# Performance work log

Measured on AMD Instinct MI355X. Metric: run time of the kernel, lower is better.

## Reference

```python
import jax, jax.numpy as jnp
import numpy as np

EPS = 1e-5  # BatchNorm eps (inference-mode BN with running stats)


def bn(x, g, b, m, v):
    # x: [B,C,H,W]; per-channel affine BN (inference)
    inv = jax.lax.rsqrt(v + EPS)
    return (x - m[None, :, None, None]) * (g * inv)[None, :, None, None] + b[None, :, None, None]


def conv1x1(x, w):
    # x: [B,Ci,H,W], w: [Co,Ci,1,1]
    return jnp.einsum('bchw,oc->bohw', x, w[:, :, 0, 0])


def conv3x3(x, w, b):
    out = jax.lax.conv_general_dilated(
        x, w, window_strides=(1, 1), padding=((1, 1), (1, 1)),
        dimension_numbers=('NCHW', 'OIHW', 'NCHW'))
    return out + b[None, :, None, None]


def deform_conv3x3(x, offset, w):
    # x: [B,C,H,W]; offset: [B,18,H,W] with channel 2k = dy_k, 2k+1 = dx_k
    # w: [Co,C,3,3]; stride=1, pad=1, dilation=1, deformable_groups=1
    B, C, H, W = x.shape
    K = 9
    kidx = jnp.arange(K)
    kdy = (kidx // 3 - 1).astype(x.dtype)  # base kernel y offsets in {-1,0,1}
    kdx = (kidx % 3 - 1).astype(x.dtype)
    off = offset.reshape(B, K, 2, H, W)
    gh = jnp.arange(H, dtype=x.dtype)
    gw = jnp.arange(W, dtype=x.dtype)
    # sampling locations [B,K,H,W]
    py = gh[None, None, :, None] + kdy[None, :, None, None] + off[:, :, 0]
    px = gw[None, None, None, :] + kdx[None, :, None, None] + off[:, :, 1]

    y0 = jnp.floor(py)
    x0 = jnp.floor(px)
    wy1 = py - y0
    wx1 = px - x0
    y0i = y0.astype(jnp.int32)
    x0i = x0.astype(jnp.int32)

    xflat = x.reshape(B, C, H * W)

    def gather(yi, xi):
        valid = ((yi >= 0) & (yi < H) & (xi >= 0) & (xi < W))
        idx = (jnp.clip(yi, 0, H - 1) * W + jnp.clip(xi, 0, W - 1)).reshape(B, 1, -1)
        g = jnp.take_along_axis(xflat, idx, axis=2).reshape(B, C, K, H, W)
        return g * valid[:, None].astype(x.dtype)

    sampled = (
        gather(y0i, x0i) * ((1 - wy1) * (1 - wx1))[:, None]
        + gather(y0i, x0i + 1) * ((1 - wy1) * wx1)[:, None]
        + gather(y0i + 1, x0i) * (wy1 * (1 - wx1))[:, None]
        + gather(y0i + 1, x0i + 1) * (wy1 * wx1)[:, None]
    )  # [B,C,K,H,W]
    return jnp.einsum('bckhw,ock->bohw', sampled, w.reshape(w.shape[0], C, K))


def setup_inputs() -> dict:
    key = jax.random.key(0)
    ks = jax.random.split(key, 20)
    B, Cin, H, W = 2, 1024, 64, 64
    Cb, Cout = 256, 1024

    def msra(k, shape):
        fan_out = shape[0] * int(np.prod(shape[2:]))
        return jax.random.normal(k, shape, jnp.float32) * np.sqrt(2.0 / fan_out)

    inp = {
        'x': jax.random.normal(ks[0], (B, Cin, H, W), jnp.float32),
        'w1': msra(ks[1], (Cb, Cin, 1, 1)),
        'g1': jnp.ones((Cb,)), 'b1': jnp.zeros((Cb,)),
        'm1': jax.random.normal(ks[2], (Cb,)) * 0.1,
        'v1': jax.random.uniform(ks[3], (Cb,)) + 0.5,
        # offset conv (small weights so offsets stay in a realistic range)
        'w_off': msra(ks[4], (18, Cb, 3, 3)) * 0.05,
        'b_off': jnp.zeros((18,)),
        'w2': msra(ks[5], (Cb, Cb, 3, 3)),
        'g2': jnp.ones((Cb,)), 'b2': jnp.zeros((Cb,)),
        'm2': jax.random.normal(ks[6], (Cb,)) * 0.1,
        'v2': jax.random.uniform(ks[7], (Cb,)) + 0.5,
        'w3': msra(ks[8], (Cout, Cb, 1, 1)),
        'g3': jnp.ones((Cout,)), 'b3': jnp.zeros((Cout,)),
        'm3': jax.random.normal(ks[9], (Cout,)) * 0.1,
        'v3': jax.random.uniform(ks[10], (Cout,)) + 0.5,
    }
    return inp


def reference(x, w1, g1, b1, m1, v1, w_off, b_off, w2, g2, b2, m2, v2,
              w3, g3, b3, m3, v3):
    out = jax.nn.relu(bn(conv1x1(x, w1), g1, b1, m1, v1))
    offset = conv3x3(out, w_off, b_off)          # [B,18,H,W]
    out = bn(deform_conv3x3(out, offset, w2), g2, b2, m2, v2)
    out = jax.nn.relu(out)
    out = bn(conv1x1(out, w3), g3, b3, m3, v3)
    out = out + x                                 # identity shortcut (Cin==Cout, stride=1)
    return jax.nn.relu(out)
```

## Files before the change

kernel.cpp:

```cpp
#include <hip/hip_runtime.h>
#include <hip/hip_bf16.h>

#define EPSV 1e-5f

typedef __attribute__((ext_vector_type(4))) float f32x4;
typedef __attribute__((ext_vector_type(8))) short bf16x8;
typedef unsigned short u16;
typedef unsigned int u32;

#define AS1(p) ((const __attribute__((address_space(1))) void*)(p))
#define AS3(p) ((__attribute__((address_space(3))) void*)(p))

__device__ __forceinline__ float bf2f(u16 u) {
    union { u32 i; float f; } x; x.i = ((u32)u) << 16; return x.f;
}
__device__ __forceinline__ u16 f2bf(float f) {
    __hip_bfloat16 h = __float2bfloat16(f);
    return *reinterpret_cast<u16*>(&h);
}

__global__ __launch_bounds__(256) void prep_all(
    const float* __restrict__ w1, const float* __restrict__ w3,
    const float* __restrict__ w_off, const float* __restrict__ w2,
    u16* __restrict__ wb1, u16* __restrict__ wb3,
    u16* __restrict__ wOffP, u16* __restrict__ wb2d,
    u16* __restrict__ zbuf)
{
    const int bz  = blockIdx.x;
    const int tid = threadIdx.x;
    if (bz < 512) {
        int i = bz * 256 + tid;
        const float* src; u16* dst; int j;
        if (i < 65536) { src = w1; dst = wb1; j = i; }
        else           { src = w3; dst = wb3; j = i - 65536; }
        float4 v = ((const float4*)src)[j];
        ushort4 o;
        o.x = f2bf(v.x); o.y = f2bf(v.y); o.z = f2bf(v.z); o.w = f2bf(v.w);
        ((ushort4*)dst)[j] = o;
        return;
    }
    const int bz1 = bz - 512;
    if (bz1 == 136) { ((u32*)zbuf)[tid] = 0; return; }
    if (bz1 < 64) {
#pragma unroll
        for (int k = 0; k < 9; k++) {
            float v = (bz1 < 18) ? w_off[((size_t)(bz1 * 256 + tid)) * 9 + k] : 0.f;
            wOffP[(size_t)bz1 * 2304 + k * 256 + tid] = f2bf(v);
        }
        return;
    }
    const int bz2 = bz1 - 64;
    const int set = bz2 % 18;
    const int kz  = bz2 / 18;
    const int tap = set >> 1, hk = set & 1;
#pragma unroll
    for (int j = 0; j < 4; j++) {
        bf16x8 ov;
#pragma unroll
        for (int kk = 0; kk < 8; kk++) {
            const int ch = kz * 64 + hk * 32 + j * 8 + kk;
            ov[kk] = (short)f2bf(w2[((size_t)(tid * 256 + ch)) * 9 + tap]);
        }
        *(bf16x8*)(wb2d + ((size_t)(bz2 * 4 + j)) * 2048 + tid * 8) = ov;
    }
}

__global__ __launch_bounds__(256) void cvt_x_T(const float* __restrict__ x,
                                               u16* __restrict__ xbT) {
    __shared__ u16 tile[64][72];
    const int tid = threadIdx.x;
    const int hw0 = blockIdx.x << 6;
    const int c0  = blockIdx.y << 6;
    const int b   = blockIdx.z;
    const int cl  = tid >> 4;
    const int hwl = (tid & 15) << 2;
#pragma unroll
    for (int i = 0; i < 4; i++) {
        const int c = cl + i * 16;
        float4 v = *(const float4*)(x + (((size_t)(b * 1024 + c0 + c)) << 12) + hw0 + hwl);
        tile[hwl + 0][c] = f2bf(v.x);
        tile[hwl + 1][c] = f2bf(v.y);
        tile[hwl + 2][c] = f2bf(v.z);
        tile[hwl + 3][c] = f2bf(v.w);
    }
    __syncthreads();
    const int hw  = tid >> 2;
    const int seg = tid & 3;
    u16* dst = xbT + ((size_t)(b * 4096 + hw0 + hw)) * 1024 + c0 + seg * 16;
    const u16* src = &tile[hw][seg * 16];
#pragma unroll
    for (int q = 0; q < 2; q++)
        *(uint4*)(dst + q * 8) = *(const uint4*)(src + q * 8);
}

#define MFMA8(ASP, BSP)                                                          \
    do {                                                                         \
        bf16x8 a0 = *(const bf16x8*)(ASP);                                       \
        bf16x8 a1 = *(const bf16x8*)((ASP) + 512);                               \
        bf16x8 b0 = *(const bf16x8*)(BSP);                                       \
        bf16x8 b1 = *(const bf16x8*)((BSP) + 512);                               \
        bf16x8 b2 = *(const bf16x8*)((BSP) + 1024);                              \
        bf16x8 b3 = *(const bf16x8*)((BSP) + 1536);                              \
        acc[0][0] = __builtin_amdgcn_mfma_f32_16x16x32_bf16(a0, b0, acc[0][0], 0, 0, 0); \
        acc[0][1] = __builtin_amdgcn_mfma_f32_16x16x32_bf16(a0, b1, acc[0][1], 0, 0, 0); \
        acc[0][2] = __builtin_amdgcn_mfma_f32_16x16x32_bf16(a0, b2, acc[0][2], 0, 0, 0); \
        acc[0][3] = __builtin_amdgcn_mfma_f32_16x16x32_bf16(a0, b3, acc[0][3], 0, 0, 0); \
        acc[1][0] = __builtin_amdgcn_mfma_f32_16x16x32_bf16(a1, b0, acc[1][0], 0, 0, 0); \
        acc[1][1] = __builtin_amdgcn_mfma_f32_16x16x32_bf16(a1, b1, acc[1][1], 0, 0, 0); \
        acc[1][2] = __builtin_amdgcn_mfma_f32_16x16x32_bf16(a1, b2, acc[1][2], 0, 0, 0); \
        acc[1][3] = __builtin_amdgcn_mfma_f32_16x16x32_bf16(a1, b3, acc[1][3], 0, 0, 0); \
    } while (0)

#define WAIT_BAR()                                  \
    do {                                            \
        asm volatile("s_waitcnt vmcnt(3)" ::: "memory"); \
        __builtin_amdgcn_s_barrier();               \
        __builtin_amdgcn_sched_barrier(0);          \
    } while (0)

#define POST_BAR()                                  \
    do {                                            \
        __builtin_amdgcn_s_barrier();               \
        __builtin_amdgcn_sched_barrier(0);          \
    } while (0)

template<int MODE>
__global__ __launch_bounds__(256) void gemm_bn(
    const u16* __restrict__ A, const u16* __restrict__ BT,
    const float* __restrict__ g, const float* __restrict__ bb,
    const float* __restrict__ m, const float* __restrict__ v,
    const float* __restrict__ resid, void* __restrict__ out, int K, int Ksub)
{
    extern __shared__ char sm[];

    const int tid  = threadIdx.x;
    const int lane = tid & 63;
    const int wid  = tid >> 6;
    const int n0 = blockIdx.x << 7;
    const int m0 = blockIdx.y << 6;
    const int kBase = blockIdx.z * Ksub;
    const int wr = wid >> 1, wc = wid & 1;
    const int lr = lane & 15, kg = lane >> 4;

    f32x4 acc[2][4] = {};

    const int arow = tid >> 2, aseg = (tid & 3) << 3;
    const u16* aG  = A  + (size_t)(m0 + arow) * K + kBase + aseg;
    const u16* bG0 = BT + (size_t)(n0 + arow) * K + kBase + aseg;
    const u16* bG1 = BT + (size_t)(n0 + 64 + arow) * K + kBase + aseg;

    char* ldsA0  = sm + wid * 1024;
    char* ldsA1  = sm + 4096  + wid * 1024;
    char* ldsB00 = sm + 8192  + wid * 1024;
    char* ldsB01 = sm + 12288 + wid * 1024;
    char* ldsB10 = sm + 16384 + wid * 1024;
    char* ldsB11 = sm + 20480 + wid * 1024;

    const u16* Asp0 = (const u16*)(sm)         + (wr * 32 + lr) * 32 + kg * 8;
    const u16* Asp1 = (const u16*)(sm + 4096)  + (wr * 32 + lr) * 32 + kg * 8;
    const u16* Bsp0 = (const u16*)(sm + 8192)  + (wc * 64 + lr) * 32 + kg * 8;
    const u16* Bsp1 = (const u16*)(sm + 16384) + (wc * 64 + lr) * 32 + kg * 8;

    float sc[2][4], tc[2][4];
#pragma unroll
    for (int mm = 0; mm < 2; mm++)
#pragma unroll
        for (int r = 0; r < 4; r++) {
            const int o = m0 + wr * 32 + mm * 16 + kg * 4 + r;
            const float s = g[o] * rsqrtf(v[o] + EPSV);
            sc[mm][r] = s;
            tc[mm][r] = bb[o] - m[o] * s;
        }
    asm volatile("s_waitcnt vmcnt(0) lgkmcnt(0)" ::: "memory");
    __builtin_amdgcn_sched_barrier(0);

#define ISSUE_G(LA, LB0, LB1, kt)                                                  \
    do {                                                                           \
        __builtin_amdgcn_global_load_lds(AS1(aG + (kt)),  AS3(LA),  16, 0, 0);     \
        __builtin_amdgcn_global_load_lds(AS1(bG0 + (kt)), AS3(LB0), 16, 0, 0);     \
        __builtin_amdgcn_global_load_lds(AS1(bG1 + (kt)), AS3(LB1), 16, 0, 0);     \
    } while (0)

    const int nT = Ksub >> 5;
    ISSUE_G(ldsA0, ldsB00, ldsB01, 0);
    ISSUE_G(ldsA1, ldsB10, ldsB11, 32);

    for (int t = 0; t < nT; t += 2) {
        WAIT_BAR();
        MFMA8(Asp0, Bsp0);
        POST_BAR();
        { const int kn = (t + 2 < nT ? t + 2 : t) << 5;
          ISSUE_G(ldsA0, ldsB00, ldsB01, kn); }
        WAIT_BAR();
        MFMA8(Asp1, Bsp1);
        POST_BAR();
        { const int kn = (t + 3 < nT ? t + 3 : t + 1) << 5;
          ISSUE_G(ldsA1, ldsB10, ldsB11, kn); }
    }
#undef ISSUE_G

    if (MODE == 1) {
        u32* T32 = (u32*)(sm + 24576);
#pragma unroll
        for (int mm = 0; mm < 2; mm++) {
            const int ol = wr * 32 + mm * 16 + kg * 4;
            const int cw0 = ol >> 1;
#pragma unroll
            for (int j = 0; j < 4; j++) {
                const int nl = wc * 64 + j * 16 + lr;
                const int sw = (nl >> 3) & 3;
                float v0 = acc[mm][j][0] * sc[mm][0] + tc[mm][0];
                float v1 = acc[mm][j][1] * sc[mm][1] + tc[mm][1];
                float v2 = acc[mm][j][2] * sc[mm][2] + tc[mm][2];
                float v3 = acc[mm][j][3] * sc[mm][3] + tc[mm][3];
                v0 = v0 > 0.f ? v0 : 0.f; v1 = v1 > 0.f ? v1 : 0.f;
                v2 = v2 > 0.f ? v2 : 0.f; v3 = v3 > 0.f ? v3 : 0.f;
                uint2 pw;
                pw.x = (u32)f2bf(v0) | ((u32)f2bf(v1) << 16);
                pw.y = (u32)f2bf(v2) | ((u32)f2bf(v3) << 16);
                *(uint2*)&T32[nl * 36 + (cw0 ^ (sw << 2))] = pw;
            }
        }
        __syncthreads();
        const int nl = tid >> 1, half = tid & 1;
        const int sw = (nl >> 3) & 3;
        u16* dst = (u16*)out + (size_t)(n0 + nl) * 256 + m0 + half * 32;
#pragma unroll
        for (int q = 0; q < 4; q++) {
            uint4 val = *(const uint4*)&T32[nl * 36 + ((half * 16 + q * 4) ^ (sw << 2))];
            *(uint4*)(dst + q * 8) = val;
        }
    } else {
        float* T = (float*)(sm + 24576);
#pragma unroll
        for (int mm = 0; mm < 2; mm++) {
            const int ol = wr * 32 + mm * 16 + kg * 4;
#pragma unroll
            for (int j = 0; j < 4; j++) {
                const int nl = wc * 64 + j * 16 + lr;
#pragma unroll
                for (int r = 0; r < 4; r++)
                    T[(ol + r) * 132 + nl] = acc[mm][j][r] * sc[mm][r] + tc[mm][r];
            }
        }
        __syncthreads();
        float* O = (float*)out;
        for (int idx = tid; idx < 2048; idx += 256) {
            const int ol  = idx >> 5;
            const int nl4 = (idx & 31) << 2;
            const int n = n0 + nl4;
            const size_t gidx = ((size_t)(n >> 12) << 22) + ((size_t)(m0 + ol) << 12) + (n & 4095);
            float4 rv = *(const float4*)(resid + gidx);
            float4 ov;
            ov.x = T[ol * 132 + nl4 + 0] + rv.x;
            ov.y = T[ol * 132 + nl4 + 1] + rv.y;
            ov.z = T[ol * 132 + nl4 + 2] + rv.z;
            ov.w = T[ol * 132 + nl4 + 3] + rv.w;
            ov.x = ov.x > 0.f ? ov.x : 0.f;
            ov.y = ov.y > 0.f ? ov.y : 0.f;
            ov.z = ov.z > 0.f ? ov.z : 0.f;
            ov.w = ov.w > 0.f ? ov.w : 0.f;
            *(float4*)(O + gidx) = ov;
        }
    }
}

__global__ __launch_bounds__(256) void gemm_off(
    const u16* __restrict__ A,
    const u16* __restrict__ out1T,
    const u16* __restrict__ zbuf,
    float* __restrict__ offsP)
{
    __shared__ char sm[24576];

    const int tid  = threadIdx.x;
    const int lane = tid & 63;
    const int wid  = tid >> 6;
    const int n0 = blockIdx.x << 7;
    const int kz = blockIdx.y;
    const int wr = wid >> 1, wc = wid & 1;
    const int lr = lane & 15, kg = lane >> 4;

    f32x4 acc[2][4] = {};

    const int arow = tid >> 2, aseg = (tid & 3) << 3;
    const u16* aG = A + (size_t)arow * 2304 + aseg;
    const int nB0 = n0 + arow, nB1 = n0 + 64 + arow;
    const int y0r = (nB0 & 4095) >> 6, x0r = nB0 & 63;
    const int y1r = (nB1 & 4095) >> 6, x1r = nB1 & 63;

    char* ldsA0  = sm + wid * 1024;
    char* ldsA1  = sm + 4096  + wid * 1024;
    char* ldsB00 = sm + 8192  + wid * 1024;
    char* ldsB01 = sm + 12288 + wid * 1024;
    char* ldsB10 = sm + 16384 + wid * 1024;
    char* ldsB11 = sm + 20480 + wid * 1024;

    const u16* Asp0 = (const u16*)(sm)         + (wr * 32 + lr) * 32 + kg * 8;
    const u16* Asp1 = (const u16*)(sm + 4096)  + (wr * 32 + lr) * 32 + kg * 8;
    const u16* Bsp0 = (const u16*)(sm + 8192)  + (wc * 64 + lr) * 32 + kg * 8;
    const u16* Bsp1 = (const u16*)(sm + 16384) + (wc * 64 + lr) * 32 + kg * 8;

#define ISSUE_O(LA, LB0, LB1, kt)                                                  \
    do {                                                                           \
        const int tap = (kt) >> 8, c0 = (kt) & 255;                                \
        const int dy = tap / 3 - 1, dx = tap % 3 - 1;                              \
        const int sh = dy * 64 + dx;                                               \
        const bool vv0 = ((unsigned)(y0r + dy) < 64u) && ((unsigned)(x0r + dx) < 64u); \
        const bool vv1 = ((unsigned)(y1r + dy) < 64u) && ((unsigned)(x1r + dx) < 64u); \
        const u16* s0 = vv0 ? out1T + (size_t)(nB0 + sh) * 256 + c0 + aseg : zbuf + aseg; \
        const u16* s1 = vv1 ? out1T + (size_t)(nB1 + sh) * 256 + c0 + aseg : zbuf + aseg; \
        __builtin_amdgcn_global_load_lds(AS1(aG + (kt)), AS3(LA),  16, 0, 0);      \
        __builtin_amdgcn_global_load_lds(AS1(s0),        AS3(LB0), 16, 0, 0);      \
        __builtin_amdgcn_global_load_lds(AS1(s1),        AS3(LB1), 16, 0, 0);      \
    } while (0)

    const int kBase = kz * 384;
    ISSUE_O(ldsA0, ldsB00, ldsB01, kBase);
    ISSUE_O(ldsA1, ldsB10, ldsB11, kBase + 32);

    for (int t = 0; t < 12; t += 2) {
        WAIT_BAR();
        MFMA8(Asp0, Bsp0);
        POST_BAR();
        { const int kn = kBase + ((t + 2 < 12 ? t + 2 : t) << 5);
          ISSUE_O(ldsA0, ldsB00, ldsB01, kn); }
        WAIT_BAR();
        MFMA8(Asp1, Bsp1);
        POST_BAR();
        { const int kn = kBase + ((t + 3 < 12 ? t + 3 : t + 1) << 5);
          ISSUE_O(ldsA1, ldsB10, ldsB11, kn); }
    }
#undef ISSUE_O

    asm volatile("s_waitcnt vmcnt(0)" ::: "memory");

#pragma unroll
    for (int mm = 0; mm < 2; mm++)
#pragma unroll
        for (int r = 0; r < 4; r++) {
            const int o = wr * 32 + mm * 16 + kg * 4 + r;
            if (o < 18) {
#pragma unroll
                for (int j = 0; j < 4; j++) {
                    const int n = n0 + wc * 64 + j * 16 + lr;
                    offsP[(size_t)kz * 147456 +
                          (((size_t)((n >> 12) * 18 + o)) << 12) + (n & 4095)] =
                        acc[mm][j][r];
                }
            }
        }
}

__global__ __launch_bounds__(256) void gemm_def(
    const u16* __restrict__ wb2d,
    const u16* __restrict__ out1T,
    const float* __restrict__ offsP,
    const float* __restrict__ b_off,
    u16* __restrict__ P)
{
    extern __shared__ char sm[];
    char*   ldsB0 = sm;
    char*   ldsB1 = sm + 4160;
    int4*   s_ofs = (int4*)(sm + 8320);
    float4* s_w   = (float4*)(sm + 17536);

    const int tid  = threadIdx.x;
    const int lane = tid & 63;
    const int wid  = tid >> 6;
    const int n0 = blockIdx.x << 6;
    const int kz = blockIdx.y;
    const int b  = n0 >> 12;
    const int h  = (n0 >> 6) & 63;
    const int lr = lane & 15, kg = lane >> 4;

    for (int p = tid; p < 576; p += 256) {
        const int t   = p >> 6;
        const int nl_ = p & 63;
        const size_t iy = (((size_t)(b * 18 + 2 * t)) << 12) + (h << 6) + nl_;
        float dy = b_off[2 * t], dx = b_off[2 * t + 1];
#pragma unroll
        for (int kzz = 0; kzz < 6; kzz++) {
            dy += offsP[(size_t)kzz * 147456 + iy];
            dx += offsP[(size_t)kzz * 147456 + iy + 4096];
        }
        const float py = (float)h + (float)(t / 3 - 1) + dy;
        const float px = (float)nl_ + (float)(t % 3 - 1) + dx;
        const float y0f = floorf(py), x0f = floorf(px);
        const int y0 = (int)y0f, x0 = (int)x0f;
        const float wy1 = py - y0f, wx1 = px - x0f;
        const float wy0 = 1.f - wy1, wx0 = 1.f - wx1;
        const int y1 = y0 + 1, x1 = x0 + 1;
        const bool vy0 = (y0 >= 0) && (y0 < 64);
        const bool vy1 = (y1 >= 0) && (y1 < 64);
        const bool vx0 = (x0 >= 0) && (x0 < 64);
        const bool vx1 = (x1 >= 0) && (x1 < 64);
        const int cy0 = min(max(y0, 0), 63), cy1 = min(max(y1, 0), 63);
        const int cx0 = min(max(x0, 0), 63), cx1 = min(max(x1, 0), 63);
        const int rb = b << 12;
        int4 o4; float4 w4;
        o4.x = (rb + (cy0 << 6) + cx0) << 9;  w4.x = wy0 * wx0 * ((vy0 && vx0) ? 1.f : 0.f);
        o4.y = (rb + (cy0 << 6) + cx1) << 9;  w4.y = wy0 * wx1 * ((vy0 && vx1) ? 1.f : 0.f);
        o4.z = (rb + (cy1 << 6) + cx0) << 9;  w4.z = wy1 * wx0 * ((vy1 && vx0) ? 1.f : 0.f);
        o4.w = (rb + (cy1 << 6) + cx1) << 9;  w4.w = wy1 * wx1 * ((vy1 && vx1) ? 1.f : 0.f);
        s_ofs[nl_ * 9 + t] = o4; s_w[nl_ * 9 + t] = w4;
    }
    __syncthreads();

    const int nl = tid >> 2;
    const int q  = tid & 3;
    const u16* aSet  = wb2d + (size_t)(kz * 18) * 8192 + kg * 2048
                            + (wid * 64 + lr) * 8;
    const char* o1B = (const char*)out1T;
    const int cbQ = kz * 128 + q * 16;

    f32x4 acc[4][4] = {};
    bf16x8 av0[4], av1[4], cr0[4], cr1[4];

#define PWC(p_) ((p_) < 18 ? (p_) : 17)

#define LOADA(RI, pt_)                                                             \
    do {                                                                           \
        const u16* ag_ = aSet + (size_t)(pt_) * 8192;                              \
        av##RI[0] = *(const bf16x8*)(ag_);                                         \
        av##RI[1] = *(const bf16x8*)(ag_ + 128);                                   \
        av##RI[2] = *(const bf16x8*)(ag_ + 256);                                   \
        av##RI[3] = *(const bf16x8*)(ag_ + 384);                                   \
    } while (0)

#define LOADC(RI, pt_)                                                             \
    do {                                                                           \
        const int tap_ = (pt_) >> 1, hk_ = (pt_) & 1;                              \
        const int4 o4_ = s_ofs[nl * 9 + tap_];                                     \
        const int cb_ = cbQ + hk_ * 64;                                            \
        cr##RI[0] = *(const bf16x8*)(o1B + o4_.x + cb_);                           \
        cr##RI[1] = *(const bf16x8*)(o1B + o4_.y + cb_);                           \
        cr##RI[2] = *(const bf16x8*)(o1B + o4_.z + cb_);                           \
        cr##RI[3] = *(const bf16x8*)(o1B + o4_.w + cb_);                           \
    } while (0)

#define PACKB(RI, LB, pw_)                                                         \
    do {                                                                           \
        const float4 w4_ = s_w[nl * 9 + ((pw_) >> 1)];                             \
        bf16x8 pk_;                                                                \
        _Pragma("unroll")                                                          \
        for (int i_ = 0; i_ < 8; i_++) {                                           \
            const float f_ = w4_.x * bf2f((u16)cr##RI[0][i_])                      \
                           + w4_.y * bf2f((u16)cr##RI[1][i_])                      \
                           + w4_.z * bf2f((u16)cr##RI[2][i_])                      \
                           + w4_.w * bf2f((u16)cr##RI[3][i_]);                     \
            pk_[i_] = (short)f2bf(f_);                                             \
        }                                                                          \
        *(bf16x8*)((LB) + q * 1040 + nl * 16) = pk_;                               \
    } while (0)

#define MFMA16(AV, LB)                                                             \
    do {                                                                           \
        bf16x8 bv0 = *(const bf16x8*)((LB) + kg * 1040 + ( 0 + lr) * 16);          \
        bf16x8 bv1 = *(const bf16x8*)((LB) + kg * 1040 + (16 + lr) * 16);          \
        bf16x8 bv2 = *(const bf16x8*)((LB) + kg * 1040 + (32 + lr) * 16);          \
        bf16x8 bv3 = *(const bf16x8*)((LB) + kg * 1040 + (48 + lr) * 16);          \
        acc[0][0] = __builtin_amdgcn_mfma_f32_16x16x32_bf16(AV[0], bv0, acc[0][0], 0, 0, 0); \
        acc[0][1] = __builtin_amdgcn_mfma_f32_16x16x32_bf16(AV[0], bv1, acc[0][1], 0, 0, 0); \
        acc[0][2] = __builtin_amdgcn_mfma_f32_16x16x32_bf16(AV[0], bv2, acc[0][2], 0, 0, 0); \
        acc[0][3] = __builtin_amdgcn_mfma_f32_16x16x32_bf16(AV[0], bv3, acc[0][3], 0, 0, 0); \
        acc[1][0] = __builtin_amdgcn_mfma_f32_16x16x32_bf16(AV[1], bv0, acc[1][0], 0, 0, 0); \
        acc[1][1] = __builtin_amdgcn_mfma_f32_16x16x32_bf16(AV[1], bv1, acc[1][1], 0, 0, 0); \
        acc[1][2] = __builtin_amdgcn_mfma_f32_16x16x32_bf16(AV[1], bv2, acc[1][2], 0, 0, 0); \
        acc[1][3] = __builtin_amdgcn_mfma_f32_16x16x32_bf16(AV[1], bv3, acc[1][3], 0, 0, 0); \
        acc[2][0] = __builtin_amdgcn_mfma_f32_16x16x32_bf16(AV[2], bv0, acc[2][0], 0, 0, 0); \
        acc[2][1] = __builtin_amdgcn_mfma_f32_16x16x32_bf16(AV[2], bv1, acc[2][1], 0, 0, 0); \
        acc[2][2] = __builtin_amdgcn_mfma_f32_16x16x32_bf16(AV[2], bv2, acc[2][2], 0, 0, 0); \
        acc[2][3] = __builtin_amdgcn_mfma_f32_16x16x32_bf16(AV[2], bv3, acc[2][3], 0, 0, 0); \
        acc[3][0] = __builtin_amdgcn_mfma_f32_16x16x32_bf16(AV[3], bv0, acc[3][0], 0, 0, 0); \
        acc[3][1] = __builtin_amdgcn_mfma_f32_16x16x32_bf16(AV[3], bv1, acc[3][1], 0, 0, 0); \
        acc[3][2] = __builtin_amdgcn_mfma_f32_16x16x32_bf16(AV[3], bv2, acc[3][2], 0, 0, 0); \
        acc[3][3] = __builtin_amdgcn_mfma_f32_16x16x32_bf16(AV[3], bv3, acc[3][3], 0, 0, 0); \
    } while (0)

#define END_BAR()                                   \
    do {                                            \
        asm volatile("s_waitcnt lgkmcnt(0)" ::: "memory"); \
        __builtin_amdgcn_s_barrier();               \
        __builtin_amdgcn_sched_barrier(0);          \
    } while (0)

    LOADC(0, 0); LOADA(0, 0);
    LOADC(1, 1); LOADA(1, 1);
    PACKB(0, ldsB0, 0);
    LOADC(0, 2);
    END_BAR();

    for (int t = 0; t < 18; t += 2) {
        PACKB(1, ldsB1, PWC(t + 1));
        LOADC(1, PWC(t + 3));
        MFMA16(av0, ldsB0);
        LOADA(0, PWC(t + 2));
        END_BAR();
        PACKB(0, ldsB0, PWC(t + 2));
        LOADC(0, PWC(t + 4));
        MFMA16(av1, ldsB1);
        LOADA(1, PWC(t + 3));
        END_BAR();
    }
#undef END_BAR
#undef MFMA16
#undef PACKB
#undef LOADC
#undef LOADA
#undef PWC

    u16* Pk = P + (size_t)kz * 2097152;
#pragma unroll
    for (int mf = 0; mf < 4; mf++)
#pragma unroll
        for (int r = 0; r < 4; r++) {
            const int o = wid * 64 + mf * 16 + kg * 4 + r;
#pragma unroll
            for (int nf = 0; nf < 4; nf++) {
                const int n = n0 + nf * 16 + lr;
                Pk[((size_t)o << 13) + n] = f2bf(acc[mf][nf][r]);
            }
        }
}

__global__ __launch_bounds__(256) void reduce_bn(
    const u16* __restrict__ P,
    const float* __restrict__ g, const float* __restrict__ bb,
    const float* __restrict__ m, const float* __restrict__ v,
    u16* __restrict__ o2T)
{
    __shared__ u16 tile[64][72];
    const int tid = threadIdx.x;
    const int n0 = blockIdx.x << 6;
    const int m0 = blockIdx.y << 6;

    const int ml = tid >> 2;
    const int ns = (tid & 3) << 4;
    const int o = m0 + ml;
    const float s = g[o] * rsqrtf(v[o] + EPSV);
    const float tcv = bb[o] - m[o] * s;
    const size_t base = ((size_t)o << 13) + n0 + ns;
#pragma unroll
    for (int qq = 0; qq < 2; qq++) {
        bf16x8 a = *(const bf16x8*)(P + base + qq * 8);
        bf16x8 b = *(const bf16x8*)(P + 2097152 + base + qq * 8);
        bf16x8 c = *(const bf16x8*)(P + 2 * 2097152 + base + qq * 8);
        bf16x8 d = *(const bf16x8*)(P + 3 * 2097152 + base + qq * 8);
#pragma unroll
        for (int i = 0; i < 8; i++) {
            float f = (bf2f((u16)a[i]) + bf2f((u16)b[i])
                     + bf2f((u16)c[i]) + bf2f((u16)d[i])) * s + tcv;
            f = f > 0.f ? f : 0.f;
            tile[ns + qq * 8 + i][ml] = f2bf(f);
        }
    }
    __syncthreads();
    const int nl = tid >> 2, seg = tid & 3;
    u16* dst = o2T + (size_t)(n0 + nl) * 256 + m0 + seg * 16;
    const u16* src = &tile[nl][seg * 16];
#pragma unroll
    for (int qq = 0; qq < 2; qq++)
        *(uint4*)(dst + qq * 8) = *(const uint4*)(src + qq * 8);
}

extern "C" void kernel_launch(void* const* d_in, const int* in_sizes, int n_in,
                              void* d_out, int out_size, void* d_ws, size_t ws_size,
                              hipStream_t stream) {
    const float* x     = (const float*)d_in[0];
    const float* w1    = (const float*)d_in[1];
    const float* g1    = (const float*)d_in[2];
    const float* b1    = (const float*)d_in[3];
    const float* m1    = (const float*)d_in[4];
    const float* v1    = (const float*)d_in[5];
    const float* w_off = (const float*)d_in[6];
    const float* b_off = (const float*)d_in[7];
    const float* w2    = (const float*)d_in[8];
    const float* g2    = (const float*)d_in[9];
    const float* b2    = (const float*)d_in[10];
    const float* m2    = (const float*)d_in[11];
    const float* v2    = (const float*)d_in[12];
    const float* w3    = (const float*)d_in[13];
    const float* g3    = (const float*)d_in[14];
    const float* b3    = (const float*)d_in[15];
    const float* m3    = (const float*)d_in[16];
    const float* v3    = (const float*)d_in[17];
    float* out = (float*)d_out;

    char* ws = (char*)d_ws;
    u16*  xbT   = (u16*)ws;   ws += (size_t)8192 * 1024 * 2;
    u16*  wb1   = (u16*)ws;   ws += (size_t)256 * 1024 * 2;
    u16*  wb3   = (u16*)ws;   ws += (size_t)1024 * 256 * 2;
    u16*  wOffP = (u16*)ws;   ws += (size_t)64 * 2304 * 2;
    u16*  wb2d  = (u16*)ws;   ws += (size_t)72 * 8192 * 2;
    u16*  zbuf  = (u16*)ws;   ws += (size_t)512 * 2;
    u16*  out1T = (u16*)ws;   ws += (size_t)8192 * 256 * 2;
    float* offsP = (float*)ws; ws += (size_t)6 * 147456 * 4;
    u16*  o2T   = (u16*)ws;   ws += (size_t)8192 * 256 * 2;
    u16*  P     = (u16*)ws;   ws += (size_t)4 * 2097152 * 2;

    prep_all<<<dim3(649), 256, 0, stream>>>(w1, w3, w_off, w2,
                                            wb1, wb3, wOffP, wb2d, zbuf);
    cvt_x_T<<<dim3(64, 16, 2), 256, 0, stream>>>(x, xbT);

    gemm_bn<1><<<dim3(64, 4), 256, 24576 + 18432, stream>>>(
        wb1, xbT, g1, b1, m1, v1, nullptr, out1T, 1024, 1024);

    gemm_off<<<dim3(64, 6), 256, 0, stream>>>(wOffP, out1T, zbuf, offsP);

    gemm_def<<<dim3(128, 4), 256, 26752, stream>>>(wb2d, out1T, offsP, b_off, P);

    reduce_bn<<<dim3(128, 4), 256, 0, stream>>>(P, g2, b2, m2, v2, o2T);

    gemm_bn<2><<<dim3(64, 16), 256, 24576 + 64 * 132 * 4, stream>>>(
        wb3, o2T, g3, b3, m3, v3, x, out, 256, 256);
}
```

Measured before the change: 92.93 us.

## Process full tap per pipeline stage in deformable GEMM, halving barriers

The deformable-conv GEMM pipeline now handles a whole kernel tap (both 64-channel halves) per stage instead of half a tap. This halves the number of LDS double-buffer stages and barriers (9 instead of 18) and issues twice as many gathers per stage for more memory-level parallelism. In exchange it doubles the register footprint for the A and gathered values and grows LDS from about 26 KB to 35 KB, which may lower occupancy.

Result: slower. 95.54 us (+2.8%).

```diff
diff --git a/kernel.cpp b/kernel.cpp
--- a/kernel.cpp
+++ b/kernel.cpp
@@ -361,9 +361,9 @@
 {
     extern __shared__ char sm[];
     char*   ldsB0 = sm;
-    char*   ldsB1 = sm + 4160;
-    int4*   s_ofs = (int4*)(sm + 8320);
-    float4* s_w   = (float4*)(sm + 17536);
+    char*   ldsB1 = sm + 8320;
+    int4*   s_ofs = (int4*)(sm + 16640);
+    float4* s_w   = (float4*)(sm + 25856);
 
     const int tid  = threadIdx.x;
     const int lane = tid & 63;
@@ -415,51 +415,64 @@
     const int cbQ = kz * 128 + q * 16;
 
     f32x4 acc[4][4] = {};
-    bf16x8 av0[4], av1[4], cr0[4], cr1[4];
-
-#define PWC(p_) ((p_) < 18 ? (p_) : 17)
-
-#define LOADA(RI, pt_)                                                             \
-    do {                                                                           \
-        const u16* ag_ = aSet + (size_t)(pt_) * 8192;                              \
-        av##RI[0] = *(const bf16x8*)(ag_);                                         \
-        av##RI[1] = *(const bf16x8*)(ag_ + 128);                                   \
-        av##RI[2] = *(const bf16x8*)(ag_ + 256);                                   \
-        av##RI[3] = *(const bf16x8*)(ag_ + 384);                                   \
-    } while (0)
-
-#define LOADC(RI, pt_)                                                             \
-    do {                                                                           \
-        const int tap_ = (pt_) >> 1, hk_ = (pt_) & 1;                              \
-        const int4 o4_ = s_ofs[nl * 9 + tap_];                                     \
-        const int cb_ = cbQ + hk_ * 64;                                            \
-        cr##RI[0] = *(const bf16x8*)(o1B + o4_.x + cb_);                           \
-        cr##RI[1] = *(const bf16x8*)(o1B + o4_.y + cb_);                           \
-        cr##RI[2] = *(const bf16x8*)(o1B + o4_.z + cb_);                           \
-        cr##RI[3] = *(const bf16x8*)(o1B + o4_.w + cb_);                           \
-    } while (0)
-
-#define PACKB(RI, LB, pw_)                                                         \
-    do {                                                                           \
-        const float4 w4_ = s_w[nl * 9 + ((pw_) >> 1)];                             \
+    bf16x8 av0a[4], av0b[4], av1a[4], av1b[4];
+    bf16x8 cr0a[4], cr0b[4], cr1a[4], cr1b[4];
+
+#define PWC(p_) ((p_) < 9 ? (p_) : 8)
+
+#define LOADA(RI, P_)                                                              \
+    do {                                                                           \
+        const u16* ag_ = aSet + (size_t)(2 * (P_)) * 8192;                         \
+        av##RI##a[0] = *(const bf16x8*)(ag_);                                      \
+        av##RI##a[1] = *(const bf16x8*)(ag_ + 128);                                \
+        av##RI##a[2] = *(const bf16x8*)(ag_ + 256);                                \
+        av##RI##a[3] = *(const bf16x8*)(ag_ + 384);                                \
+        av##RI##b[0] = *(const bf16x8*)(ag_ + 8192);                               \
+        av##RI##b[1] = *(const bf16x8*)(ag_ + 8320);                               \
+        av##RI##b[2] = *(const bf16x8*)(ag_ + 8448);                               \
+        av##RI##b[3] = *(const bf16x8*)(ag_ + 8576);                               \
+    } while (0)
+
+#define LOADC(RI, P_)                                                              \
+    do {                                                                           \
+        const int4 o4_ = s_ofs[nl * 9 + (P_)];                                     \
+        cr##RI##a[0] = *(const bf16x8*)(o1B + o4_.x + cbQ);                        \
+        cr##RI##a[1] = *(const bf16x8*)(o1B + o4_.y + cbQ);                        \
+        cr##RI##a[2] = *(const bf16x8*)(o1B + o4_.z + cbQ);                        \
+        cr##RI##a[3] = *(const bf16x8*)(o1B + o4_.w + cbQ);                        \
+        cr##RI##b[0] = *(const bf16x8*)(o1B + o4_.x + cbQ + 64);                   \
+        cr##RI##b[1] = *(const bf16x8*)(o1B + o4_.y + cbQ + 64);                   \
+        cr##RI##b[2] = *(const bf16x8*)(o1B + o4_.z + cbQ + 64);                   \
+        cr##RI##b[3] = *(const bf16x8*)(o1B + o4_.w + cbQ + 64);                   \
+    } while (0)
+
+#define PACK1(CR, LBP)                                                             \
+    do {                                                                           \
         bf16x8 pk_;                                                                \
         _Pragma("unroll")                                                          \
         for (int i_ = 0; i_ < 8; i_++) {                                           \
-            const float f_ = w4_.x * bf2f((u16)cr##RI[0][i_])                      \
-                           + w4_.y * bf2f((u16)cr##RI[1][i_])                      \
-                           + w4_.z * bf2f((u16)cr##RI[2][i_])                      \
-                           + w4_.w * bf2f((u16)cr##RI[3][i_]);                     \
+            const float f_ = w4_.x * bf2f((u16)CR[0][i_])                          \
+                           + w4_.y * bf2f((u16)CR[1][i_])                          \
+                           + w4_.z * bf2f((u16)CR[2][i_])                          \
+                           + w4_.w * bf2f((u16)CR[3][i_]);                         \
             pk_[i_] = (short)f2bf(f_);                                             \
         }                                                                          \
-        *(bf16x8*)((LB) + q * 1040 + nl * 16) = pk_;                               \
-    } while (0)
-
-#define MFMA16(AV, LB)                                                             \
-    do {                                                                           \
-        bf16x8 bv0 = *(const bf16x8*)((LB) + kg * 1040 + ( 0 + lr) * 16);          \
-        bf16x8 bv1 = *(const bf16x8*)((LB) + kg * 1040 + (16 + lr) * 16);          \
-        bf16x8 bv2 = *(const bf16x8*)((LB) + kg * 1040 + (32 + lr) * 16);          \
-        bf16x8 bv3 = *(const bf16x8*)((LB) + kg * 1040 + (48 + lr) * 16);          \
+        *(bf16x8*)(LBP) = pk_;                                                     \
+    } while (0)
+
+#define PACKB(RI, LB, P_)                                                          \
+    do {                                                                           \
+        const float4 w4_ = s_w[nl * 9 + (P_)];                                     \
+        PACK1(cr##RI##a, (LB) + q * 1040 + nl * 16);                               \
+        PACK1(cr##RI##b, (LB) + 4160 + q * 1040 + nl * 16);                        \
+    } while (0)
+
+#define MFMA16S(AV, LBS)                                                           \
+    do {                                                                           \
+        bf16x8 bv0 = *(const bf16x8*)((LBS) + kg * 1040 + ( 0 + lr) * 16);         \
+        bf16x8 bv1 = *(const bf16x8*)((LBS) + kg * 1040 + (16 + lr) * 16);         \
+        bf16x8 bv2 = *(const bf16x8*)((LBS) + kg * 1040 + (32 + lr) * 16);         \
+        bf16x8 bv3 = *(const bf16x8*)((LBS) + kg * 1040 + (48 + lr) * 16);         \
         acc[0][0] = __builtin_amdgcn_mfma_f32_16x16x32_bf16(AV[0], bv0, acc[0][0], 0, 0, 0); \
         acc[0][1] = __builtin_amdgcn_mfma_f32_16x16x32_bf16(AV[0], bv1, acc[0][1], 0, 0, 0); \
         acc[0][2] = __builtin_amdgcn_mfma_f32_16x16x32_bf16(AV[0], bv2, acc[0][2], 0, 0, 0); \
@@ -478,6 +491,12 @@
         acc[3][3] = __builtin_amdgcn_mfma_f32_16x16x32_bf16(AV[3], bv3, acc[3][3], 0, 0, 0); \
     } while (0)
 
+#define MFMA32(RI, LB)                                                             \
+    do {                                                                           \
+        MFMA16S(av##RI##a, (LB));                                                  \
+        MFMA16S(av##RI##b, (LB) + 4160);                                           \
+    } while (0)
+
 #define END_BAR()                                   \
     do {                                            \
         asm volatile("s_waitcnt lgkmcnt(0)" ::: "memory"); \
@@ -491,21 +510,24 @@
     LOADC(0, 2);
     END_BAR();
 
-    for (int t = 0; t < 18; t += 2) {
+    for (int t = 0; t < 8; t += 2) {
         PACKB(1, ldsB1, PWC(t + 1));
         LOADC(1, PWC(t + 3));
-        MFMA16(av0, ldsB0);
+        MFMA32(0, ldsB0);
         LOADA(0, PWC(t + 2));
         END_BAR();
         PACKB(0, ldsB0, PWC(t + 2));
         LOADC(0, PWC(t + 4));
-        MFMA16(av1, ldsB1);
+        MFMA32(1, ldsB1);
         LOADA(1, PWC(t + 3));
         END_BAR();
     }
+    MFMA32(0, ldsB0);
 #undef END_BAR
-#undef MFMA16
+#undef MFMA32
+#undef MFMA16S
 #undef PACKB
+#undef PACK1
 #undef LOADC
 #undef LOADA
 #undef PWC
@@ -608,7 +630,7 @@
 
     gemm_off<<<dim3(64, 6), 256, 0, stream>>>(wOffP, out1T, zbuf, offsP);
 
-    gemm_def<<<dim3(128, 4), 256, 26752, stream>>>(wb2d, out1T, offsP, b_off, P);
+    gemm_def<<<dim3(128, 4), 256, 35072, stream>>>(wb2d, out1T, offsP, b_off, P);
 
     reduce_bn<<<dim3(128, 4), 256, 0, stream>>>(P, g2, b2, m2, v2, o2T);
 
```
